# Kernel optimization log

Measured on AMD Instinct MI355X. Metric: run time of the kernel, lower is better.

The kernel has to match this reference:

```python
import jax, jax.numpy as jnp
import numpy as np

RR = 16
PFRAC = 0.5
GMAX = 1.0
GMIN = 0.0
TAU = 50.0
SPKRANGE = 128
H = W = 128


def setup_inputs() -> dict:
    key = jax.random.key(0)
    k1, k2, k3, k4, k5 = jax.random.split(key, 5)
    SN = 32
    xy = jax.random.randint(k1, (SN, SPKRANGE, 2), 0, 128)          # x, y pixel coords
    pol = jax.random.randint(k2, (SN, SPKRANGE, 1), 0, 2)           # polarity channel
    dt = jax.random.uniform(k3, (SN, SPKRANGE), minval=1.0, maxval=20.0)
    t = jnp.cumsum(dt, axis=1)                                      # increasing timestamps
    event = jnp.concatenate(
        [xy.astype(jnp.float32), pol.astype(jnp.float32), t[..., None]], axis=-1
    )                                                               # (SN, S, 4): x, y, p, t
    time_trace = jax.random.randint(k4, (SN, SPKRANGE), 0, RR)
    length = jax.random.randint(k5, (SN,), 1, SPKRANGE)
    return {"event": event, "time_trace": time_trace, "length": length, "test": 0}


def _te_forward(event, time_trace, length):
    SN = event.shape[0]
    coords = event[..., :3].astype(jnp.int32)   # (SN, S, 3): x, y, polarity
    times = event[..., 3]                        # (SN, S)
    s_idx = jnp.arange(SN)

    T2G = jnp.zeros((SN, RR, 2, H, W), dtype=event.dtype)
    # initial spike deposited into frame 0
    x0, y0, p0 = coords[:, 0, 0], coords[:, 0, 1], coords[:, 0, 2]
    T2G = T2G.at[s_idx, 0, p0, x0, y0].add(PFRAC * (GMAX - GMIN))

    # time-major stacked scan inputs for steps N = 1 .. SPKRANGE-1
    tt_prev = time_trace[:, :-1].T               # (S-1, SN)
    tt_cur = time_trace[:, 1:].T                 # (S-1, SN)
    c_cur = jnp.transpose(coords[:, 1:], (1, 0, 2))  # (S-1, SN, 3)
    dts = (times[:, :-1] - times[:, 1:]).T       # t_{N-1} - t_N  (negative)
    alive = (length[None, :] >= jnp.arange(1, SPKRANGE)[:, None]).astype(event.dtype)

    def step(T2G, xs):
        ttp, ttc, cN, d, a = xs
        MM = jnp.exp(d / TAU)                    # (SN,) per-sample decay factor
        prev = T2G[s_idx, ttp]                   # gather (SN, 2, H, W) slices
        new = MM[:, None, None, None] * (prev - GMIN) + GMIN
        x, y, p = cN[:, 0], cN[:, 1], cN[:, 2]
        cur = new[s_idx, p, x, y]                # value after overwrite, as in torch
        new = new.at[s_idx, p, x, y].add(a * PFRAC * (GMAX - cur))
        T2G = T2G.at[s_idx, ttc].set(new)        # scatter full slices back
        return T2G, None

    T2G, _ = jax.lax.scan(step, T2G, (tt_prev, tt_cur, c_cur, dts, alive))
    return T2G


def reference(event, time_trace, length, test):
    T2G = _te_forward(event, time_trace, length)
    side = 76 if test == 1 else 96               # CenterCrop(76) for test, 96 for train
    off = (H - side) // 2
    return T2G[:, :, :, off:off + side, off:off + side]
```

## Files before the change

### kernel.cpp

```cpp
#include <hip/hip_runtime.h>
#include <math.h>

#define SN   32
#define RR_  16
#define SPK  128
#define NZB  32


__global__ __launch_bounds__(256) void te_plane(
    const float* __restrict__ event,
    const int*   __restrict__ time_trace,
    const int*   __restrict__ length_,
    float*       __restrict__ out,
    int side)
{
    const int b = blockIdx.x;
    const int s = b / NZB;
    const int c = b % NZB;
    const int r = c >> 1, p = c & 1;
    const int t = threadIdx.x;
    const int plane = side * side;

    __shared__ int   ids[SPK];
    __shared__ int   uu[SPK];
    __shared__ float mm[SPK];
    __shared__ int   tt[SPK];
    __shared__ float tms[SPK];

    float* o = out + (size_t)b * (size_t)plane;
    {
        float4 z4 = make_float4(0.f, 0.f, 0.f, 0.f);
        float4* o4 = (float4*)o;
        const int n4 = plane >> 2;
        for (int k = t; k < n4; k += 256) o4[k] = z4;
    }

    const float4* ev = (const float4*)(event + (size_t)s * SPK * 4);
    for (int i = t; i < SPK; i += 256) {
        float4 e = ev[i];
        ids[i] = (((int)e.z) << 14) | (((int)e.x) << 7) | ((int)e.y);
        tms[i] = e.w;
        tt[i]  = time_trace[s * SPK + i];
    }
    __syncthreads();

    if (t < SPK) {
        int id = ids[t];
        int u = t;
        for (int j = 0; j < t; ++j) {
            if (ids[j] == id) { u = j; break; }
        }
        uu[t] = u;
        if (t >= 1) {
            double d = (double)tms[t - 1] - (double)tms[t];
            mm[t] = (float)exp(d / 50.0);
        }
    }
    __syncthreads();

    float vr = 0.0f;
    bool  own = false;
    int   xo = 0, yo = 0;
    if (t < SPK) {
        const int e   = t;
        const int len = length_[s];
        float v = (tt[0] == 0 && e == 0) ? 0.5f : 0.0f;
        vr      = (r == 0     && e == 0) ? 0.5f : 0.0f;
        if (tt[0] == r) vr = v;
        for (int i = 1; i < SPK; ++i) {
            v = v * mm[i];
            if ((len >= i) && (uu[i] == e))
                v = v + 0.5f * (1.0f - v);
            if (tt[i] == r) vr = v;
        }
        if (uu[t] == t) {
            int id = ids[t];
            if (((id >> 14) & 1) == p) {
                int y = id & 127, x = (id >> 7) & 127;
                int off = (128 - side) / 2;
                xo = x - off; yo = y - off;
                own = (xo >= 0 && xo < side && yo >= 0 && yo < side);
            }
        }
    }

    __syncthreads();

    if (own) o[xo * side + yo] = vr;
}

extern "C" void kernel_launch(void* const* d_in, const int* in_sizes, int n_in,
                              void* d_out, int out_size, void* d_ws, size_t ws_size,
                              hipStream_t stream) {
    const float* event      = (const float*)d_in[0];
    const int*   time_trace = (const int*)d_in[1];
    const int*   length_    = (const int*)d_in[2];
    float*       out        = (float*)d_out;

    const int side = (out_size == SN * RR_ * 2 * 76 * 76) ? 76 : 96;

    te_plane<<<SN * NZB, 256, 0, stream>>>(event, time_trace, length_, out, side);
}
```

Baseline: 89.14 us.

## Split decay simulation into one per-sample kernel plus a separate plane-fill kernel

Previously each of the 1024 blocks, one per (sample, frame, polarity), re-ran the full 127-step per-event decay simulation and duplicate-coordinate search. The new te_sim kernel runs that simulation once per sample. It records each event's value for every frame in shared memory and writes a compact value table and deduplicated ids to workspace. A second kernel, te_fill, only zeroes each output plane and scatters the precomputed values. This removes the redundant serial work per plane, at the cost of an extra launch, a workspace round-trip, and a small 32-block serial stage that uses few CUs.

```diff
diff --git a/kernel.cpp b/kernel.cpp
--- a/kernel.cpp
+++ b/kernel.cpp
@@ -7,12 +7,65 @@
 #define NZB  32
 
 
-__global__ __launch_bounds__(256) void te_plane(
+__global__ __launch_bounds__(128) void te_sim(
     const float* __restrict__ event,
     const int*   __restrict__ time_trace,
     const int*   __restrict__ length_,
-    float*       __restrict__ out,
-    int side)
+    float*       __restrict__ ws_val,
+    int*         __restrict__ ws_id)
+{
+    const int s = blockIdx.x;
+    const int t = threadIdx.x;
+
+    __shared__ int   ids[SPK];
+    __shared__ int   uu[SPK];
+    __shared__ float mm[SPK];
+    __shared__ int   tt[SPK];
+    __shared__ float tms[SPK];
+    __shared__ float val[RR_ * SPK];
+
+    const float4 e = ((const float4*)(event + (size_t)s * SPK * 4))[t];
+    ids[t] = (((int)e.z) << 14) | (((int)e.x) << 7) | ((int)e.y);
+    tms[t] = e.w;
+    tt[t]  = time_trace[s * SPK + t];
+    for (int k = t; k < RR_ * SPK; k += 128) val[k] = 0.0f;
+    __syncthreads();
+
+    {
+        const int id = ids[t];
+        int u = t;
+        for (int j = t - 1; j >= 0; --j)
+            if (ids[j] == id) u = j;
+        uu[t] = u;
+        if (t >= 1) {
+            double d = (double)tms[t - 1] - (double)tms[t];
+            mm[t] = (float)exp(d / 50.0);
+        }
+    }
+    if (t == 0) val[0 * SPK + 0] = 0.5f;
+    __syncthreads();
+
+    {
+        const int len = length_[s];
+        float v = (tt[0] == 0 && t == 0) ? 0.5f : 0.0f;
+        for (int i = 1; i < SPK; ++i) {
+            v = v * mm[i];
+            if ((len >= i) && (uu[i] == t))
+                v = v + 0.5f * (1.0f - v);
+            val[tt[i] * SPK + t] = v;
+        }
+    }
+    __syncthreads();
+
+    for (int k = t; k < RR_ * SPK; k += 128)
+        ws_val[(size_t)s * RR_ * SPK + k] = val[k];
+    ws_id[s * SPK + t] = (uu[t] == t) ? ids[t] : -1;
+}
+
+__global__ __launch_bounds__(256) void te_fill(
+    const float* __restrict__ ws_val,
+    const int*   __restrict__ ws_id,
+    float*       __restrict__ out, int side)
 {
     const int b = blockIdx.x;
     const int s = b / NZB;
@@ -21,72 +74,32 @@
     const int t = threadIdx.x;
     const int plane = side * side;
 
-    __shared__ int   ids[SPK];
-    __shared__ int   uu[SPK];
-    __shared__ float mm[SPK];
-    __shared__ int   tt[SPK];
-    __shared__ float tms[SPK];
+    float* o = out + (size_t)b * (size_t)plane;
 
-    float* o = out + (size_t)b * (size_t)plane;
-    {
-        float4 z4 = make_float4(0.f, 0.f, 0.f, 0.f);
-        float4* o4 = (float4*)o;
-        const int n4 = plane >> 2;
-        for (int k = t; k < n4; k += 256) o4[k] = z4;
+    int   id = -1;
+    float v  = 0.0f;
+    if (t < SPK) {
+        id = ws_id[s * SPK + t];
+        if (id >= 0 && ((id >> 14) & 1) == p)
+            v = ws_val[((size_t)s * RR_ + r) * SPK + t];
+        else
+            id = -1;
     }
 
-    const float4* ev = (const float4*)(event + (size_t)s * SPK * 4);
-    for (int i = t; i < SPK; i += 256) {
-        float4 e = ev[i];
-        ids[i] = (((int)e.z) << 14) | (((int)e.x) << 7) | ((int)e.y);
-        tms[i] = e.w;
-        tt[i]  = time_trace[s * SPK + i];
-    }
-    __syncthreads();
-
-    if (t < SPK) {
-        int id = ids[t];
-        int u = t;
-        for (int j = 0; j < t; ++j) {
-            if (ids[j] == id) { u = j; break; }
-        }
-        uu[t] = u;
-        if (t >= 1) {
-            double d = (double)tms[t - 1] - (double)tms[t];
-            mm[t] = (float)exp(d / 50.0);
-        }
-    }
-    __syncthreads();
-
-    float vr = 0.0f;
-    bool  own = false;
-    int   xo = 0, yo = 0;
-    if (t < SPK) {
-        const int e   = t;
-        const int len = length_[s];
-        float v = (tt[0] == 0 && e == 0) ? 0.5f : 0.0f;
-        vr      = (r == 0     && e == 0) ? 0.5f : 0.0f;
-        if (tt[0] == r) vr = v;
-        for (int i = 1; i < SPK; ++i) {
-            v = v * mm[i];
-            if ((len >= i) && (uu[i] == e))
-                v = v + 0.5f * (1.0f - v);
-            if (tt[i] == r) vr = v;
-        }
-        if (uu[t] == t) {
-            int id = ids[t];
-            if (((id >> 14) & 1) == p) {
-                int y = id & 127, x = (id >> 7) & 127;
-                int off = (128 - side) / 2;
-                xo = x - off; yo = y - off;
-                own = (xo >= 0 && xo < side && yo >= 0 && yo < side);
-            }
-        }
-    }
+    float4  z4 = make_float4(0.f, 0.f, 0.f, 0.f);
+    float4* o4 = (float4*)o;
+    const int n4 = plane >> 2;
+    for (int k = t; k < n4; k += 256) o4[k] = z4;
 
     __syncthreads();
 
-    if (own) o[xo * side + yo] = vr;
+    if (id >= 0) {
+        int y = id & 127, x = (id >> 7) & 127;
+        int off = (128 - side) / 2;
+        int xo = x - off, yo = y - off;
+        if (xo >= 0 && xo < side && yo >= 0 && yo < side)
+            o[xo * side + yo] = v;
+    }
 }
 
 extern "C" void kernel_launch(void* const* d_in, const int* in_sizes, int n_in,
@@ -99,5 +112,10 @@
 
     const int side = (out_size == SN * RR_ * 2 * 76 * 76) ? 76 : 96;
 
-    te_plane<<<SN * NZB, 256, 0, stream>>>(event, time_trace, length_, out, side);
+    float* ws_val = (float*)d_ws;
+    int*   ws_id  = (int*)((char*)d_ws + (size_t)SN * RR_ * SPK * sizeof(float));
+
+    te_sim <<<SN,       128, 0, stream>>>(event, time_trace, length_,
+                                          ws_val, ws_id);
+    te_fill<<<SN * NZB, 256, 0, stream>>>(ws_val, ws_id, out, side);
 }
```

Result: no change. 87.42 us (-1.9%).
